# Optimization experiments

Hardware: AMD Instinct MI355X
Metric: run time of the kernel (lower is better)

The kernel has to match this reference:

```python
import jax, jax.numpy as jnp
import numpy as np

DS = 8  # downsample_factor


def learned_upflow(flow, mask, ds=DS):
    """Convex-combination upsampling, faithful to Model.learned_upflow.

    flow: (n, 2, h, w)   coarse flow at 1/ds resolution
    mask: (n, 9*ds*ds, h, w)  raw (pre-softmax) convex weights
    returns: (n, 2, ds*h, ds*w)
    """
    n, _, h, w = flow.shape
    # mask.view(n, 1, 9, ds, ds, h, w); softmax over the 9 neighbor taps
    m = mask.reshape(n, 1, 9, ds, ds, h, w)
    m = jax.nn.softmax(m, axis=2)

    # F.unfold(ds*flow, [3,3], padding=1) -> 3x3 neighborhoods, row-major
    # kernel order (dy outer, dx inner), channel-major — matches the
    # subsequent view(n, 2, 9, 1, 1, h, w).
    fp = jnp.pad(ds * flow, ((0, 0), (0, 0), (1, 1), (1, 1)))
    patches = jnp.stack(
        [fp[:, :, dy:dy + h, dx:dx + w] for dy in range(3) for dx in range(3)],
        axis=2,
    )  # (n, 2, 9, h, w)

    up = jnp.sum(m * patches[:, :, :, None, None, :, :], axis=2)  # (n,2,ds,ds,h,w)
    # permute(0,1,4,2,5,3) then reshape -> (n, 2, ds*h, ds*w)
    up = up.transpose(0, 1, 4, 2, 5, 3)
    return up.reshape(n, 2, ds * h, ds * w)


def setup_inputs() -> dict:
    key = jax.random.key(0)
    k1, k2 = jax.random.split(key)
    n, h, w = 4, 136, 240
    flow = jax.random.normal(k1, (n, 2, h, w), dtype=jnp.float32)
    mask = jax.random.normal(k2, (n, 9 * DS * DS, h, w), dtype=jnp.float32)
    return {"flow": flow, "mask": mask}


def reference(flow, mask):
    return learned_upflow(flow, mask)
```

## Files before the change

### kernel.cpp

```cpp
#include <hip/hip_runtime.h>

#define HH 136
#define WW 240
#define HW (HH * WW)
#define DS 8
#define OW (DS * WW)
#define OH (DS * HH)
#define CROWS 18
#define NCH 4

typedef float vf4 __attribute__((ext_vector_type(4)));

__device__ __forceinline__ void gload_lds16(const float* g, float* l) {
  __builtin_amdgcn_global_load_lds(
      (const __attribute__((address_space(1))) void*)g,
      (__attribute__((address_space(3))) void*)l, 16, 0, 0);
}

__global__ __launch_bounds__(256, 7) void upflow_kernel(
    const float* __restrict__ flow,
    const float* __restrict__ mask,
    float* __restrict__ out) {
  __shared__ float lm[CROWS][WW];

  int h = blockIdx.x;
  int ni = blockIdx.y;
  int i = ni & 7;
  int n = ni >> 3;
  int tid = threadIdx.x;
  int wid = tid >> 6, lane = tid & 63;
  int px = tid;
  bool stager = lane < 60;

  const float* mrow = mask + ((size_t)n * 576 + i * 8) * HW + (size_t)h * WW;

  float f0[9], f1[9];
  if (px < WW) {
    const float* fb0 = flow + (size_t)(n * 2 + 0) * HW;
    const float* fb1 = flow + (size_t)(n * 2 + 1) * HW;
#pragma unroll
    for (int dy = 0; dy < 3; ++dy) {
      int hh = h + dy - 1;
      bool rok = (hh >= 0) && (hh < HH);
#pragma unroll
      for (int dx = 0; dx < 3; ++dx) {
        int k = dy * 3 + dx;
        int cc = px + dx - 1;
        bool ok = rok && (cc >= 0) && (cc < WW);
        int idx = hh * WW + cc;
        f0[k] = ok ? 8.0f * fb0[idx] : 0.0f;
        f1[k] = ok ? 8.0f * fb1[idx] : 0.0f;
      }
    }
  }

  const float L2E = 1.4426950408889634f;
  float sj[8], d0j[8], d1j[8];
#pragma unroll
  for (int j = 0; j < 8; ++j) { sj[j] = 0.f; d0j[j] = 0.f; d1j[j] = 0.f; }

#pragma unroll
  for (int c = 0; c < NCH; ++c) {
    if (stager) {
#pragma unroll
      for (int t = 0; t < 5; ++t) {
        int rr = wid + 4 * t;
        if (rr < CROWS) {
          int g = c * CROWS + rr;
          const float* src =
              mrow + (size_t)((g >> 3) * 64 + (g & 7)) * HW + lane * 4;
          gload_lds16(src, &lm[rr][0]);
        }
      }
    }
    __syncthreads();
    if (px < WW) {
#pragma unroll
      for (int rr = 0; rr < CROWS; ++rr) {
        const int g = c * CROWS + rr;
        const int k = g >> 3, j = g & 7;
        float e = exp2f(lm[rr][px] * L2E);
        sj[j] += e;
        d0j[j] += e * f0[k];
        d1j[j] += e * f1[k];
      }
    }
    if (c < NCH - 1) __syncthreads();
  }

  if (px < WW) {
    size_t ob0 =
        ((size_t)(n * 2 + 0) * OH + (size_t)(h * 8 + i)) * (size_t)OW + px * 8;
    size_t ob1 = ob0 + (size_t)OH * OW;
    float r0 = 1.0f / sj[0], r1 = 1.0f / sj[1], r2 = 1.0f / sj[2],
          r3 = 1.0f / sj[3], r4 = 1.0f / sj[4], r5 = 1.0f / sj[5],
          r6 = 1.0f / sj[6], r7 = 1.0f / sj[7];
    vf4 a = {d0j[0] * r0, d0j[1] * r1, d0j[2] * r2, d0j[3] * r3};
    vf4 b = {d0j[4] * r4, d0j[5] * r5, d0j[6] * r6, d0j[7] * r7};
    vf4 c = {d1j[0] * r0, d1j[1] * r1, d1j[2] * r2, d1j[3] * r3};
    vf4 d = {d1j[4] * r4, d1j[5] * r5, d1j[6] * r6, d1j[7] * r7};
    *(vf4*)(out + ob0) = a;
    *(vf4*)(out + ob0 + 4) = b;
    *(vf4*)(out + ob1) = c;
    *(vf4*)(out + ob1 + 4) = d;
  }
}

extern "C" void kernel_launch(void* const* d_in, const int* in_sizes, int n_in,
                              void* d_out, int out_size, void* d_ws, size_t ws_size,
                              hipStream_t stream) {
  const float* flow = (const float*)d_in[0];
  const float* mask = (const float*)d_in[1];
  float* out = (float*)d_out;
  dim3 grid(HH, 32);
  upflow_kernel<<<grid, 256, 0, stream>>>(flow, mask, out);
}
```

Baseline: 76.72 us.

## Double-buffer mask rows in LDS with async prefetch of next chunk

Splits the per-block mask rows into six chunks of twelve rows instead of four of eighteen. It double-buffers them in LDS so the global-to-LDS DMA for chunk c+1 is issued before computing on chunk c. Explicit s_waitcnt vmcnt and raw s_barrier calls replace __syncthreads so only the current chunk's loads are awaited. The aim is to hide memory latency behind the exp/accumulate work, at the cost of doubled LDS footprint, which may reduce occupancy, and fragile manual vmcnt accounting.

```diff
diff --git a/kernel.cpp b/kernel.cpp
--- a/kernel.cpp
+++ b/kernel.cpp
@@ -6,8 +6,8 @@
 #define DS 8
 #define OW (DS * WW)
 #define OH (DS * HH)
-#define CROWS 18
-#define NCH 4
+#define CROWS 12
+#define NCH 6
 
 typedef float vf4 __attribute__((ext_vector_type(4)));
 
@@ -21,7 +21,7 @@
     const float* __restrict__ flow,
     const float* __restrict__ mask,
     float* __restrict__ out) {
-  __shared__ float lm[CROWS][WW];
+  __shared__ float lm[2][CROWS][WW];
 
   int h = blockIdx.x;
   int ni = blockIdx.y;
@@ -33,6 +33,15 @@
   bool stager = lane < 60;
 
   const float* mrow = mask + ((size_t)n * 576 + i * 8) * HW + (size_t)h * WW;
+
+  if (stager) {
+#pragma unroll
+    for (int t = 0; t < 3; ++t) {
+      int rr = wid + 4 * t;
+      gload_lds16(mrow + (size_t)((rr >> 3) * 64 + (rr & 7)) * HW + lane * 4,
+                  &lm[0][rr][0]);
+    }
+  }
 
   float f0[9], f1[9];
   if (px < WW) {
@@ -61,31 +70,41 @@
 
 #pragma unroll
   for (int c = 0; c < NCH; ++c) {
-    if (stager) {
+    if (c + 1 < NCH) {
+      if (stager) {
 #pragma unroll
-      for (int t = 0; t < 5; ++t) {
-        int rr = wid + 4 * t;
-        if (rr < CROWS) {
-          int g = c * CROWS + rr;
-          const float* src =
-              mrow + (size_t)((g >> 3) * 64 + (g & 7)) * HW + lane * 4;
-          gload_lds16(src, &lm[rr][0]);
+        for (int t = 0; t < 3; ++t) {
+          int rr = wid + 4 * t;
+          int g = (c + 1) * CROWS + rr;
+          gload_lds16(
+              mrow + (size_t)((g >> 3) * 64 + (g & 7)) * HW + lane * 4,
+              &lm[(c + 1) & 1][rr][0]);
         }
       }
+      asm volatile("s_waitcnt vmcnt(3)" ::: "memory");
+    } else {
+      asm volatile("s_waitcnt vmcnt(0)" ::: "memory");
     }
-    __syncthreads();
+    __builtin_amdgcn_s_barrier();
+    asm volatile("" ::: "memory");
+
     if (px < WW) {
 #pragma unroll
       for (int rr = 0; rr < CROWS; ++rr) {
         const int g = c * CROWS + rr;
         const int k = g >> 3, j = g & 7;
-        float e = exp2f(lm[rr][px] * L2E);
+        float e = exp2f(lm[c & 1][rr][px] * L2E);
         sj[j] += e;
         d0j[j] += e * f0[k];
         d1j[j] += e * f1[k];
       }
     }
-    if (c < NCH - 1) __syncthreads();
+
+    if (c + 1 < NCH) {
+      asm volatile("" ::: "memory");
+      __builtin_amdgcn_s_barrier();
+      asm volatile("" ::: "memory");
+    }
   }
 
   if (px < WW) {
```

After: 74.66 us. 2.7% less time.
